# Performance work log

Measured on AMD Instinct MI355X. Metric: run time of the kernel, lower is better.

The kernel has to match this reference:

```python
import jax, jax.numpy as jnp
import numpy as np

NNZ = 4_194_304
IN_FEATURES = 4096
OUT_FEATURES = 4096
BATCH = 4
SEQ = 2048


def setup_inputs() -> dict:
    key = jax.random.key(0)
    k1, k2, k3, k4, k5, k6 = jax.random.split(key, 6)
    x = jax.random.normal(k1, (BATCH, SEQ, IN_FEATURES), dtype=jnp.float32)
    rows = jax.random.randint(k2, (NNZ,), 0, OUT_FEATURES, dtype=jnp.int32)
    cols = jax.random.randint(k3, (NNZ,), 0, IN_FEATURES, dtype=jnp.int32)
    w_real = jax.random.normal(k4, (NNZ,), dtype=jnp.float32)
    w_imag = jax.random.normal(k5, (NNZ,), dtype=jnp.float32)
    phase_angles = jax.random.uniform(k6, (BATCH,), dtype=jnp.float32) * 2.0 * np.pi
    return {
        "x": x,
        "rows": rows,
        "cols": cols,
        "w_real": w_real,
        "w_imag": w_imag,
        "phase_angles": phase_angles,
        "out_features": OUT_FEATURES,
    }


def reference(x, rows, cols, w_real, w_imag, phase_angles, out_features):
    B, S, F_in = x.shape
    N = B * S
    x_flat = x.reshape(N, F_in)  # [N, F_in]
    # per-flattened-row cosine phase (phase is per-batch, repeated over seq)
    cos_p = jnp.cos(jnp.repeat(phase_angles, S))  # [N]
    # assemble sparse COO weights into dense (out, in) matrices (duplicates sum)
    Wr = jnp.zeros((out_features, F_in), dtype=x_flat.dtype).at[rows, cols].add(w_real)
    Wi = jnp.zeros((out_features, F_in), dtype=x_flat.dtype).at[rows, cols].add(w_imag)
    # out[n, r] = sum_e x[n, cols[e]] * (w_real[e] + cos(phase[n]) * w_imag[e])
    out = x_flat @ Wr.T + cos_p[:, None] * (x_flat @ Wi.T)  # [N, out]
    return out.reshape(B, S, out_features)
```

## Files before the change

### kernel.cpp

```cpp
#include <hip/hip_runtime.h>


#define K_IN   4096
#define F_OUT  4096
#define SEQ    2048
#define NROW   8192
#define NNZ    4194304
#define WELEM  16777216
#define NBUCK  1024
#define SEGB   5120

typedef float  f32x4  __attribute__((ext_vector_type(4)));
typedef __bf16 bf16x8 __attribute__((ext_vector_type(8)));
typedef unsigned short u16x8 __attribute__((ext_vector_type(8)));

__device__ __forceinline__ unsigned short f2bf(float f) {
  unsigned u = __builtin_bit_cast(unsigned, f);
  u += 0x7fffu + ((u >> 16) & 1u);
  return (unsigned short)(u >> 16);
}
__device__ __forceinline__ float bf2f(unsigned short b) {
  return __builtin_bit_cast(float, (unsigned)b << 16);
}

__global__ __launch_bounds__(1024) void bin_kernel(
    const int* __restrict__ rows, const int* __restrict__ cols,
    const float* __restrict__ wre, const float* __restrict__ wim,
    unsigned* __restrict__ cursor, unsigned long long* __restrict__ records,
    const float* __restrict__ x, unsigned short* __restrict__ Xb) {
  const int b = blockIdx.x;
  if (b < 256) {
    __shared__ unsigned cnt[NBUCK];
    const int tid = threadIdx.x;
    const int e0 = b << 14;
    cnt[tid] = 0u;
    __syncthreads();
    #pragma unroll
    for (int i = 0; i < 16; ++i)
      atomicAdd(&cnt[((unsigned)rows[e0 + (i << 10) + tid]) >> 2], 1u);
    __syncthreads();
    {
      const unsigned c = cnt[tid];
      unsigned base = 0u;
      if (c) base = atomicAdd(&cursor[tid], c);
      cnt[tid] = base;
    }
    __syncthreads();
    for (int i = 0; i < 16; ++i) {
      const int e = e0 + (i << 10) + tid;
      const unsigned r  = (unsigned)rows[e];
      const unsigned bk = r >> 2;
      const unsigned rank = atomicAdd(&cnt[bk], 1u);
      const unsigned pk = (unsigned)f2bf(wre[e]) | ((unsigned)f2bf(wim[e]) << 16);
      if (rank < SEGB)
        records[(size_t)bk * SEGB + rank] =
            ((unsigned long long)pk << 32) | ((r & 3u) << 12) | (unsigned)cols[e];
    }
  } else {
    const size_t i8 = (((size_t)(b - 256) << 10) + threadIdx.x) << 3;
    f32x4 a = *(const f32x4*)(x + i8);
    f32x4 c = *(const f32x4*)(x + i8 + 4);
    u16x8 v;
    v[0] = f2bf(a[0]); v[1] = f2bf(a[1]); v[2] = f2bf(a[2]); v[3] = f2bf(a[3]);
    v[4] = f2bf(c[0]); v[5] = f2bf(c[1]); v[6] = f2bf(c[2]); v[7] = f2bf(c[3]);
    *(u16x8*)(Xb + i8) = v;
  }
}

__global__ __launch_bounds__(1024) void assemble_kernel(
    const unsigned* __restrict__ cursor,
    const unsigned long long* __restrict__ records,
    const float* __restrict__ phase, unsigned short* __restrict__ Wb) {
  __shared__ float accRe[16384];
  __shared__ float accIm[16384];
  const int bk  = blockIdx.x;
  const int tid = threadIdx.x;
  #pragma unroll
  for (int i = 0; i < 16; ++i) {
    accRe[(i << 10) + tid] = 0.f;
    accIm[(i << 10) + tid] = 0.f;
  }
  __syncthreads();
  unsigned cnt = cursor[bk];
  if (cnt > SEGB) cnt = SEGB;
  const unsigned long long* seg = records + (size_t)bk * SEGB;
  for (unsigned i = tid; i < cnt; i += 1024) {
    const unsigned long long rec = seg[i];
    const unsigned s = (unsigned)rec & 16383u;
    atomicAdd(&accRe[s], bf2f((unsigned short)((rec >> 32) & 0xffffu)));
    atomicAdd(&accIm[s], bf2f((unsigned short)(rec >> 48)));
  }
  __syncthreads();
  float cb[4];
  cb[0] = cosf(phase[0]); cb[1] = cosf(phase[1]);
  cb[2] = cosf(phase[2]); cb[3] = cosf(phase[3]);
  #pragma unroll
  for (int it = 0; it < 16; ++it) {
    const int s = (it << 10) + tid;
    const float re = accRe[s];
    const float im = accIm[s];
    #pragma unroll
    for (int bb = 0; bb < 4; ++bb)
      Wb[((size_t)bb << 24) + ((size_t)bk << 14) + s] = f2bf(re + cb[bb] * im);
  }
}

#define GLOAD_LDS(g, l)                                                        \
  __builtin_amdgcn_global_load_lds(                                            \
      (const __attribute__((address_space(1))) unsigned int*)(g),              \
      (__attribute__((address_space(3))) unsigned int*)(l), 16, 0, 0)

__global__ __launch_bounds__(512, 2) void gemm_kernel(
    const unsigned short* __restrict__ Xb,
    const unsigned short* __restrict__ Wb,
    float* __restrict__ out) {
  __shared__ unsigned short lds[65536];

  const int tid  = threadIdx.x;
  const int wid  = tid >> 6;
  const int lane = tid & 63;
  const int wr   = wid >> 2;
  const int wc   = wid & 3;

  const int bid  = blockIdx.x;
  const int swz  = ((bid & 7) << 6) | (bid >> 3);
  const int brow = swz >> 4;
  const int bcol = swz & 15;
  const size_t M0 = (size_t)brow << 8;
  const int batch = brow >> 3;
  const unsigned short* Ap = Xb + M0 * K_IN;
  const unsigned short* Bp = Wb + ((size_t)batch << 24) + (((size_t)bcol << 8) * K_IN);

  const int srow4 = lane >> 2;
  const int gsl   = (((lane & 3) ^ ((lane >> 2) & 3) ^ ((lane >> 4) & 3)) << 3);
  const int lrow = lane & 15;
  const int sb   = lane >> 4;
  const int fsl  = ((sb ^ (lrow & 3) ^ ((lrow >> 2) & 3)) << 3);

  f32x4 acc[8][4] = {};

#define STAGE(buf, kt)                                                         \
  {                                                                            \
    _Pragma("unroll")                                                          \
    for (int l = 0; l < 2; ++l) {                                              \
      const int rb = (l << 7) + (wid << 4);                                    \
      GLOAD_LDS(Ap + (size_t)(rb + srow4) * K_IN + (size_t)(((kt) << 5) + gsl),\
                &lds[((buf) << 14) + (rb << 5)]);                              \
    }                                                                          \
    _Pragma("unroll")                                                          \
    for (int l = 0; l < 2; ++l) {                                              \
      const int rb = (l << 7) + (wid << 4);                                    \
      GLOAD_LDS(Bp + (size_t)(rb + srow4) * K_IN + (size_t)(((kt) << 5) + gsl),\
                &lds[((buf) << 14) + 8192 + (rb << 5)]);                       \
    }                                                                          \
  }

#define COMPUTE(buf)                                                           \
  {                                                                            \
    const unsigned short* la = &lds[(buf) << 14];                              \
    const unsigned short* lb = la + 8192;                                      \
    bf16x8 af[8], bff[4];                                                      \
    _Pragma("unroll")                                                          \
    for (int m = 0; m < 8; ++m)                                                \
      af[m] = *(const bf16x8*)&la[(((wr << 7) + (m << 4) + lrow) << 5) + fsl]; \
    _Pragma("unroll")                                                          \
    for (int n = 0; n < 4; ++n)                                                \
      bff[n] = *(const bf16x8*)&lb[(((wc << 6) + (n << 4) + lrow) << 5) + fsl];\
    __builtin_amdgcn_s_setprio(1);                                             \
    _Pragma("unroll")                                                          \
    for (int m = 0; m < 8; ++m)                                                \
      _Pragma("unroll")                                                        \
      for (int n = 0; n < 4; ++n)                                              \
        acc[m][n] = __builtin_amdgcn_mfma_f32_16x16x32_bf16(                   \
            af[m], bff[n], acc[m][n], 0, 0, 0);                                \
    __builtin_amdgcn_s_setprio(0);                                             \
  }

#define STEP(cb, sbuf, kt)                                                     \
  {                                                                            \
    STAGE(sbuf, kt);                                                           \
    asm volatile("s_waitcnt vmcnt(12)\n\ts_barrier" ::: "memory");             \
    COMPUTE(cb);                                                               \
    asm volatile("s_waitcnt lgkmcnt(0)\n\ts_barrier" ::: "memory");            \
  }

  STAGE(0, 0); STAGE(1, 1); STAGE(2, 2);
  for (int I = 0; I < 31; ++I) {
    const int t = I << 2;
    STEP(0, 3, t + 3); STEP(1, 0, t + 4); STEP(2, 1, t + 5); STEP(3, 2, t + 6);
  }
  STEP(0, 3, 127);
  asm volatile("s_waitcnt vmcnt(8)\n\ts_barrier" ::: "memory");
  COMPUTE(1);
  asm volatile("s_waitcnt lgkmcnt(0)\n\ts_barrier" ::: "memory");
  asm volatile("s_waitcnt vmcnt(4)\n\ts_barrier" ::: "memory");
  COMPUTE(2);
  asm volatile("s_waitcnt lgkmcnt(0)\n\ts_barrier" ::: "memory");
  asm volatile("s_waitcnt vmcnt(0)\n\ts_barrier" ::: "memory");
  COMPUTE(3);

  const int ch = lane >> 4;
  float* op = out + (M0 + (size_t)(wr << 7)) * F_OUT + ((size_t)bcol << 8) + (wc << 6);
  #pragma unroll
  for (int m = 0; m < 8; ++m)
    #pragma unroll
    for (int n = 0; n < 4; ++n)
      #pragma unroll
      for (int j = 0; j < 4; ++j)
        op[(size_t)((m << 4) + (ch << 2) + j) * F_OUT + (n << 4) + lrow] = acc[m][n][j];
#undef STAGE
#undef COMPUTE
#undef STEP
}

__global__ __launch_bounds__(256) void scatter_kernel(
    const int* __restrict__ rows, const int* __restrict__ cols,
    const float* __restrict__ wre, const float* __restrict__ wim,
    unsigned short* __restrict__ Wcb) {
  int e = blockIdx.x * 256 + threadIdx.x;
  int r = rows[e];
  int c = cols[e];
  unsigned pk = (unsigned)f2bf(wre[e]) | ((unsigned)f2bf(wim[e]) << 16);
  size_t idx = ((size_t)r << 12) + (size_t)c;
  asm volatile("global_atomic_pk_add_bf16 %0, %1, off"
               :: "v"(Wcb + (idx << 1)), "v"(pk) : "memory");
}
__global__ __launch_bounds__(256) void fold_kernel(
    const unsigned short* __restrict__ Wcb, const float* __restrict__ phase,
    unsigned short* __restrict__ Wb) {
  size_t i8 = ((size_t)blockIdx.x * 256 + threadIdx.x) << 3;
  float cb[4];
  cb[0] = cosf(phase[0]); cb[1] = cosf(phase[1]);
  cb[2] = cosf(phase[2]); cb[3] = cosf(phase[3]);
  const unsigned short* p = Wcb + (i8 << 1);
  u16x8 a = *(const u16x8*)(p);
  u16x8 b = *(const u16x8*)(p + 8);
  float rr[8], ii[8];
  rr[0] = bf2f(a[0]); ii[0] = bf2f(a[1]);
  rr[1] = bf2f(a[2]); ii[1] = bf2f(a[3]);
  rr[2] = bf2f(a[4]); ii[2] = bf2f(a[5]);
  rr[3] = bf2f(a[6]); ii[3] = bf2f(a[7]);
  rr[4] = bf2f(b[0]); ii[4] = bf2f(b[1]);
  rr[5] = bf2f(b[2]); ii[5] = bf2f(b[3]);
  rr[6] = bf2f(b[4]); ii[6] = bf2f(b[5]);
  rr[7] = bf2f(b[6]); ii[7] = bf2f(b[7]);
  #pragma unroll
  for (int bb = 0; bb < 4; ++bb) {
    float c = cb[bb];
    u16x8 v;
    #pragma unroll
    for (int j = 0; j < 8; ++j) v[j] = f2bf(rr[j] + c * ii[j]);
    *(u16x8*)(Wb + ((size_t)bb << 24) + i8) = v;
  }
}
__global__ __launch_bounds__(256) void xconv_kernel(
    const float* __restrict__ x, unsigned short* __restrict__ Xb) {
  size_t i8 = ((size_t)blockIdx.x * 256 + threadIdx.x) << 3;
  f32x4 a = *(const f32x4*)(x + i8);
  f32x4 c = *(const f32x4*)(x + i8 + 4);
  u16x8 v;
  v[0] = f2bf(a[0]); v[1] = f2bf(a[1]); v[2] = f2bf(a[2]); v[3] = f2bf(a[3]);
  v[4] = f2bf(c[0]); v[5] = f2bf(c[1]); v[6] = f2bf(c[2]); v[7] = f2bf(c[3]);
  *(u16x8*)(Xb + i8) = v;
}
__global__ __launch_bounds__(256) void naive_kernel(
    const float* __restrict__ x, const unsigned short* __restrict__ Wcb,
    const float* __restrict__ phase, float* __restrict__ out) {
  int n = blockIdx.x >> 4;
  int r = ((blockIdx.x & 15) << 8) | threadIdx.x;
  float cb = cosf(phase[n >> 11]);
  const float* xp = x + ((size_t)n << 12);
  const unsigned short* wc = Wcb + (((size_t)r << 12) << 1);
  float ar = 0.f, ai = 0.f;
  for (int k = 0; k < K_IN; ++k) {
    float xv = xp[k];
    ar += xv * bf2f(wc[2 * k]);
    ai += xv * bf2f(wc[2 * k + 1]);
  }
  out[((size_t)n << 12) + r] = ar + cb * ai;
}

extern "C" void kernel_launch(void* const* d_in, const int* in_sizes, int n_in,
                              void* d_out, int out_size, void* d_ws, size_t ws_size,
                              hipStream_t stream) {
  const float* x     = (const float*)d_in[0];
  const int*   rows  = (const int*)d_in[1];
  const int*   cols  = (const int*)d_in[2];
  const float* wre   = (const float*)d_in[3];
  const float* wim   = (const float*)d_in[4];
  const float* phase = (const float*)d_in[5];
  float* out = (float*)d_out;

  const size_t WS_FULL = (size_t)268435456;
  const size_t WS_MAIN = (size_t)201326592;
  if (ws_size >= WS_FULL) {
    unsigned short*     Wb      = (unsigned short*)d_ws;
    unsigned short*     Xb      = (unsigned short*)((char*)d_ws + (size_t)134217728);
    unsigned long long* records = (unsigned long long*)((char*)d_ws + (size_t)201326592);
    unsigned*           cursor  = (unsigned*)((char*)d_ws + (size_t)251658240);
    hipMemsetAsync(cursor, 0, NBUCK * sizeof(unsigned), stream);
    bin_kernel<<<256 + 4096, 1024, 0, stream>>>(rows, cols, wre, wim,
                                                cursor, records, x, Xb);
    assemble_kernel<<<NBUCK, 1024, 0, stream>>>(cursor, records, phase, Wb);
    gemm_kernel<<<512, 512, 0, stream>>>(Xb, Wb, out);
  } else if (ws_size >= WS_MAIN) {
    unsigned short* Wcb = (unsigned short*)d_ws;
    unsigned short* Wb  = (unsigned short*)((char*)d_ws + (size_t)67108864);
    unsigned short* Xb  = (unsigned short*)d_ws;
    hipMemsetAsync(d_ws, 0, (size_t)WELEM * 4, stream);
    scatter_kernel<<<NNZ / 256, 256, 0, stream>>>(rows, cols, wre, wim, Wcb);
    fold_kernel<<<WELEM / 8 / 256, 256, 0, stream>>>(Wcb, phase, Wb);
    xconv_kernel<<<(size_t)NROW * K_IN / 8 / 256, 256, 0, stream>>>(x, Xb);
    gemm_kernel<<<512, 512, 0, stream>>>(Xb, Wb, out);
  } else {
    unsigned short* Wcb = (unsigned short*)d_ws;
    hipMemsetAsync(d_ws, 0, (size_t)WELEM * 4, stream);
    scatter_kernel<<<NNZ / 256, 256, 0, stream>>>(rows, cols, wre, wim, Wcb);
    naive_kernel<<<NROW * 16, 256, 0, stream>>>(x, Wcb, phase, out);
  }
}
```

Measured before the change: 446.6 us.

## Stage binned records in shared memory before coalesced global scatter

```diff
diff --git a/kernel.cpp b/kernel.cpp
--- a/kernel.cpp
+++ b/kernel.cpp
@@ -28,9 +28,12 @@
     const float* __restrict__ wre, const float* __restrict__ wim,
     unsigned* __restrict__ cursor, unsigned long long* __restrict__ records,
     const float* __restrict__ x, unsigned short* __restrict__ Xb) {
+  __shared__ unsigned long long sorted[16384];
+  __shared__ unsigned cnt[NBUCK];
+  __shared__ unsigned loff[NBUCK];
+  __shared__ unsigned gbase[NBUCK];
   const int b = blockIdx.x;
   if (b < 256) {
-    __shared__ unsigned cnt[NBUCK];
     const int tid = threadIdx.x;
     const int e0 = b << 14;
     cnt[tid] = 0u;
@@ -39,22 +42,40 @@
     for (int i = 0; i < 16; ++i)
       atomicAdd(&cnt[((unsigned)rows[e0 + (i << 10) + tid]) >> 2], 1u);
     __syncthreads();
-    {
-      const unsigned c = cnt[tid];
-      unsigned base = 0u;
-      if (c) base = atomicAdd(&cursor[tid], c);
-      cnt[tid] = base;
+    const unsigned c0 = cnt[tid];
+    gbase[tid] = c0 ? atomicAdd(&cursor[tid], c0) : 0u;
+    loff[tid] = c0;
+    __syncthreads();
+    #pragma unroll
+    for (int d = 1; d < 1024; d <<= 1) {
+      const unsigned v = loff[tid];
+      const unsigned a = (tid >= d) ? loff[tid - d] : 0u;
+      __syncthreads();
+      loff[tid] = v + a;
+      __syncthreads();
     }
+    const unsigned excl = loff[tid] - c0;
+    loff[tid] = excl;
+    cnt[tid]  = excl;
     __syncthreads();
     for (int i = 0; i < 16; ++i) {
       const int e = e0 + (i << 10) + tid;
       const unsigned r  = (unsigned)rows[e];
       const unsigned bk = r >> 2;
-      const unsigned rank = atomicAdd(&cnt[bk], 1u);
+      const unsigned lr = atomicAdd(&cnt[bk], 1u);
       const unsigned pk = (unsigned)f2bf(wre[e]) | ((unsigned)f2bf(wim[e]) << 16);
-      if (rank < SEGB)
-        records[(size_t)bk * SEGB + rank] =
-            ((unsigned long long)pk << 32) | ((r & 3u) << 12) | (unsigned)cols[e];
+      sorted[lr] = ((unsigned long long)pk << 32) |
+                   ((unsigned long long)bk << 14) |
+                   ((r & 3u) << 12) | (unsigned)cols[e];
+    }
+    __syncthreads();
+    #pragma unroll
+    for (int i = 0; i < 16; ++i) {
+      const int idx = (i << 10) + tid;
+      const unsigned long long v = sorted[idx];
+      const unsigned bk = (unsigned)(v >> 14) & 1023u;
+      const unsigned dst = gbase[bk] + ((unsigned)idx - loff[bk]);
+      if (dst < SEGB) records[(size_t)bk * SEGB + dst] = v;
     }
   } else {
     const size_t i8 = (((size_t)(b - 256) << 10) + threadIdx.x) << 3;
```

Measured after the change: 413.0 us. 1.08x faster.
